# Kernel tuning notes

Hardware: AMD Instinct MI355X
Metric: run time of the kernel (lower is better)

Reference implementation:

```python
import jax, jax.numpy as jnp
import numpy as np

SOM_H, SOM_W = 16, 16
K = SOM_H * SOM_W          # num_embeddings = 256
EMB_D = 32                 # embedding_dim
ALPHA, BETA = 6.0, 1.0


def _build_tables():
    """Static SOM grid neighbor tables (rectangular geometry).
    ind[k] is a 0/1 row over the K codebook entries marking k and its
    up/down/left/right grid neighbors; counts[k] = number of neighbors incl self.
    Replaces the original per-voxel Python loop with a constant lookup table.
    """
    ind = np.zeros((K, K), np.float32)
    for idx in range(K):
        h, w = divmod(idx, SOM_W)
        neigh = [idx]
        if h - 1 >= 0:
            neigh.append((h - 1) * SOM_W + w)
        if h + 1 < SOM_H:
            neigh.append((h + 1) * SOM_W + w)
        if w - 1 >= 0:
            neigh.append(h * SOM_W + (w - 1))
        if w + 1 < SOM_W:
            neigh.append(h * SOM_W + (w + 1))
        ind[idx, neigh] = 1.0
    counts = ind.sum(axis=1)
    return jnp.asarray(ind), jnp.asarray(counts)

_IND_TABLE, _COUNTS = _build_tables()


def setup_inputs() -> dict:
    key = jax.random.key(0)
    k1, k2 = jax.random.split(key)
    x = jax.random.normal(k1, (8, EMB_D, 32, 32, 32), dtype=jnp.float32)  # [B,C,D,H,W]
    W = jax.random.normal(k2, (K, EMB_D), dtype=jnp.float32)              # codebook
    return {"x": x, "W": W}


def reference(x, W):
    # channels-last: [B, D, H, Wd, C]
    inputs = jnp.transpose(x, (0, 2, 3, 4, 1))
    in_shape = inputs.shape
    flat = inputs.reshape(-1, EMB_D)                    # [N, d]
    flat_sg = jax.lax.stop_gradient(flat)               # matches flat_inputs.detach()

    # squared Euclidean distances to all codebook entries: [N, K]
    dist = (jnp.sum(flat_sg ** 2, axis=1, keepdims=True)
            + jnp.sum(W ** 2, axis=1)
            - 2.0 * flat_sg @ W.T)

    enc_idx = jnp.argmin(dist, axis=1)                  # [N]
    encodings = jax.nn.one_hot(enc_idx, K, dtype=inputs.dtype)  # [N, K]

    quantized = (encodings @ W).reshape(in_shape)
    commitment_loss = jnp.mean((quantized - inputs) ** 2)

    # vectorized neighbor indicator + counts via static table gather
    indicator = _IND_TABLE[enc_idx]                     # [N, K], constant wrt floats
    total_neighbors = jnp.sum(_COUNTS[enc_idx])
    somloss = jnp.sum(dist * indicator) / total_neighbors

    loss = ALPHA * commitment_loss + BETA * somloss

    # straight-through estimator
    quantized_st = inputs + jax.lax.stop_gradient(quantized - inputs)
    out = jnp.transpose(quantized_st, (0, 4, 1, 2, 3))  # back to [B,C,D,H,W]
    return loss, out, encodings
```

## Files before the change

### kernel.cpp

```cpp
#include <hip/hip_runtime.h>


#define SOM_K      256
#define EMB_D      32
#define WPAD       36
#define N_VOX      262144
#define SPATIAL    32768
#define OUT_ELEMS  8388608
#define COMMIT_DEN 8388608.0f
#define NSLOT      256

#define CONST_AS __attribute__((address_space(4)))

__global__ __launch_bounds__(256) void som_prep_kernel(float* __restrict__ ws) {
  float4* p = (float4*)ws;
  int t = threadIdx.x;
#pragma unroll
  for (int i = 0; i < 4; ++i) p[i * 256 + t] = make_float4(0.f, 0.f, 0.f, 0.f);
}

__global__ __launch_bounds__(256, 4) void som_main_kernel(
    const float* __restrict__ x,
    const float* __restrict__ w,
    float* __restrict__ slots,
    float* __restrict__ out,
    float* __restrict__ enc) {
  __shared__ __align__(16) float wl[SOM_K * WPAD];
  __shared__ __align__(16) float wsql[SOM_K];

  const int t = threadIdx.x;
  const CONST_AS float* wcp = (const CONST_AS float*)(unsigned long long)w;

  const int n    = blockIdx.x * 256 + t;
  const int base = (n >> 15) * (EMB_D * SPATIAL) + (n & (SPATIAL - 1));
  float xv[EMB_D];
#pragma unroll
  for (int c = 0; c < EMB_D; ++c) xv[c] = x[base + c * SPATIAL];

#pragma unroll
  for (int i = 0; i < 32; ++i) {
    int e = i * 256 + t;
    int r = e >> 5, c = e & 31;
    wl[r * WPAD + c] = w[e];
  }
  __syncthreads();

  {
    const float4* row = (const float4*)(wl + t * WPAD);
    float s = 0.0f;
#pragma unroll
    for (int j = 0; j < 8; ++j) {
      float4 q = row[j];
      s = fmaf(q.x, q.x, s);
      s = fmaf(q.y, q.y, s);
      s = fmaf(q.z, q.z, s);
      s = fmaf(q.w, q.w, s);
    }
    wsql[t] = s;
  }

  float xsq = 0.0f;
#pragma unroll
  for (int c = 0; c < EMB_D; ++c) xsq = fmaf(xv[c], xv[c], xsq);
  __syncthreads();

  {
    const int lane = t & 63, wave = t >> 6;
    float* rb = enc + (size_t)(blockIdx.x * 256 + wave * 64) * SOM_K;
    float4* rb4 = (float4*)(rb + 3);
    const float4 z4 = make_float4(0.f, 0.f, 0.f, 0.f);
    for (int r = 0; r < 63; ++r) rb4[r * 64 + lane] = z4;
    if (lane < 63) rb4[4032 + lane] = z4;
    if (lane == 0)       { rb[0] = 0.f; rb[1] = 0.f; rb[2] = 0.f; }
    else if (lane == 63) { rb[16383] = 0.f; }
  }

  float best = 3.402823466e38f;
  int   bidx = 0;
  const float4* wsq4 = (const float4*)wsql;
#pragma unroll 1
  for (int k = 0; k < SOM_K; k += 4) {
    const CONST_AS float* r0 = wcp + (k << 5);
    const CONST_AS float* r1 = r0 + 32;
    const CONST_AS float* r2 = r0 + 64;
    const CONST_AS float* r3 = r0 + 96;
    float d0 = 0.0f, d1 = 0.0f, d2 = 0.0f, d3 = 0.0f;
#pragma unroll
    for (int j = 0; j < EMB_D; ++j) {
      const float xj = xv[j];
      d0 = fmaf(r0[j], xj, d0);
      d1 = fmaf(r1[j], xj, d1);
      d2 = fmaf(r2[j], xj, d2);
      d3 = fmaf(r3[j], xj, d3);
    }
    const float4 ws4 = wsq4[k >> 2];
    const float e0 = (xsq + ws4.x) - 2.0f * d0;
    const float e1 = (xsq + ws4.y) - 2.0f * d1;
    const float e2 = (xsq + ws4.z) - 2.0f * d2;
    const float e3 = (xsq + ws4.w) - 2.0f * d3;
    if (e0 < best) { best = e0; bidx = k;     }
    if (e1 < best) { best = e1; bidx = k + 1; }
    if (e2 < best) { best = e2; bidx = k + 2; }
    if (e3 < best) { best = e3; bidx = k + 3; }
  }

  asm volatile("s_waitcnt vmcnt(0)" ::: "memory");
  enc[(size_t)n * SOM_K + bidx] = 1.0f;

  float commit = 0.0f;
  {
    const float4* qrow = (const float4*)(wl + bidx * WPAD);
#pragma unroll
    for (int j = 0; j < 8; ++j) {
      float4 q = qrow[j];
      float qq[4] = { q.x, q.y, q.z, q.w };
#pragma unroll
      for (int u = 0; u < 4; ++u) {
        int c = 4 * j + u;
        out[base + c * SPATIAL] = qq[u];
        float df = qq[u] - xv[c];
        commit = fmaf(df, df, commit);
      }
    }
  }

  float som = best;
  float cnt = 1.0f;
  {
    const int h   = bidx >> 4;
    const int wc2 = bidx & 15;
    const int   cand[4]  = { bidx - 16, bidx + 16, bidx - 1, bidx + 1 };
    const float valid[4] = { h > 0 ? 1.f : 0.f,  h < 15 ? 1.f : 0.f,
                             wc2 > 0 ? 1.f : 0.f, wc2 < 15 ? 1.f : 0.f };
#pragma unroll
    for (int j = 0; j < 4; ++j) {
      int nk = valid[j] != 0.0f ? cand[j] : bidx;
      const float4* nrow = (const float4*)(wl + nk * WPAD);
      float dot = 0.0f;
#pragma unroll
      for (int jj = 0; jj < 8; ++jj) {
        float4 q = nrow[jj];
        dot = fmaf(q.x, xv[4 * jj + 0], dot);
        dot = fmaf(q.y, xv[4 * jj + 1], dot);
        dot = fmaf(q.z, xv[4 * jj + 2], dot);
        dot = fmaf(q.w, xv[4 * jj + 3], dot);
      }
      float d = (xsq + wsql[nk]) - 2.0f * dot;
      som = fmaf(valid[j], d, som);
      cnt += valid[j];
    }
  }

  for (int off = 32; off > 0; off >>= 1) {
    commit += __shfl_down(commit, off, 64);
    som    += __shfl_down(som,    off, 64);
    cnt    += __shfl_down(cnt,    off, 64);
  }
  if ((t & 63) == 0) {
    float* sp = slots + (size_t)(blockIdx.x & (NSLOT - 1)) * 16;
    atomicAdd(sp + 0, commit);
    atomicAdd(sp + 1, som);
    atomicAdd(sp + 2, cnt);
  }
}

__global__ __launch_bounds__(64) void som_final_kernel(
    const float* __restrict__ slots, float* __restrict__ loss) {
  const int t = threadIdx.x;
  float commit = 0.f, som = 0.f, cnt = 0.f;
#pragma unroll
  for (int i = 0; i < 4; ++i) {
    const float* sp = slots + (size_t)(i * 64 + t) * 16;
    commit += sp[0]; som += sp[1]; cnt += sp[2];
  }
  for (int off = 32; off > 0; off >>= 1) {
    commit += __shfl_down(commit, off, 64);
    som    += __shfl_down(som,    off, 64);
    cnt    += __shfl_down(cnt,    off, 64);
  }
  if (t == 0) loss[0] = 6.0f * (commit / COMMIT_DEN) + som / cnt;
}

extern "C" void kernel_launch(void* const* d_in, const int* in_sizes, int n_in,
                              void* d_out, int out_size, void* d_ws, size_t ws_size,
                              hipStream_t stream) {
  const float* x = (const float*)d_in[0];
  const float* w = (const float*)d_in[1];
  float* ws  = (float*)d_ws;
  float* o   = (float*)d_out;

  som_prep_kernel<<<1, 256, 0, stream>>>(ws);
  som_main_kernel<<<N_VOX / 256, 256, 0, stream>>>(
      x, w, ws, o + 1, o + 1 + OUT_ELEMS);
  som_final_kernel<<<1, 64, 0, stream>>>(ws, o);
}
```

Measured before the change: 402.7 us.

## Split each voxel's codebook search across two threads and drop the LDS codebook copy

Each block now runs 512 threads, and each voxel is handled by a thread pair. Each thread of the pair scans half of the 256 codebook entries, and the two results are merged with a lane shuffle that breaks ties toward the lower index. The shared-memory copy of the codebook is removed; the quantized row and the SOM neighbor distances are read directly from global memory, with the neighbor work and output channels split between the two threads. The aim is more parallelism and shorter per-thread argmin loops. The cost is that codebook reads no longer use the constant/scalar address space and become per-lane vector memory loads, and both threads of a pair load the full input vector.

```diff
diff --git a/kernel.cpp b/kernel.cpp
--- a/kernel.cpp
+++ b/kernel.cpp
@@ -3,15 +3,12 @@
 
 #define SOM_K      256
 #define EMB_D      32
-#define WPAD       36
 #define N_VOX      262144
 #define SPATIAL    32768
 #define OUT_ELEMS  8388608
 #define COMMIT_DEN 8388608.0f
 #define NSLOT      256
 
-#define CONST_AS __attribute__((address_space(4)))
-
 __global__ __launch_bounds__(256) void som_prep_kernel(float* __restrict__ ws) {
   float4* p = (float4*)ws;
   int t = threadIdx.x;
@@ -19,42 +16,30 @@
   for (int i = 0; i < 4; ++i) p[i * 256 + t] = make_float4(0.f, 0.f, 0.f, 0.f);
 }
 
-__global__ __launch_bounds__(256, 4) void som_main_kernel(
+__global__ __launch_bounds__(512, 8) void som_main_kernel(
     const float* __restrict__ x,
     const float* __restrict__ w,
     float* __restrict__ slots,
     float* __restrict__ out,
     float* __restrict__ enc) {
-  __shared__ __align__(16) float wl[SOM_K * WPAD];
   __shared__ __align__(16) float wsql[SOM_K];
 
-  const int t = threadIdx.x;
-  const CONST_AS float* wcp = (const CONST_AS float*)(unsigned long long)w;
-
-  const int n    = blockIdx.x * 256 + t;
+  const int t    = threadIdx.x;
+  const int half = t & 1;
+  const int vloc = t >> 1;
+  const int n    = blockIdx.x * 256 + vloc;
   const int base = (n >> 15) * (EMB_D * SPATIAL) + (n & (SPATIAL - 1));
+
   float xv[EMB_D];
 #pragma unroll
   for (int c = 0; c < EMB_D; ++c) xv[c] = x[base + c * SPATIAL];
 
-#pragma unroll
-  for (int i = 0; i < 32; ++i) {
-    int e = i * 256 + t;
-    int r = e >> 5, c = e & 31;
-    wl[r * WPAD + c] = w[e];
-  }
-  __syncthreads();
-
-  {
-    const float4* row = (const float4*)(wl + t * WPAD);
+  if (t < SOM_K) {
     float s = 0.0f;
 #pragma unroll
-    for (int j = 0; j < 8; ++j) {
-      float4 q = row[j];
-      s = fmaf(q.x, q.x, s);
-      s = fmaf(q.y, q.y, s);
-      s = fmaf(q.z, q.z, s);
-      s = fmaf(q.w, q.w, s);
+    for (int c = 0; c < EMB_D; ++c) {
+      float v = w[t * EMB_D + c];
+      s = fmaf(v, v, s);
     }
     wsql[t] = s;
   }
@@ -66,24 +51,28 @@
 
   {
     const int lane = t & 63, wave = t >> 6;
-    float* rb = enc + (size_t)(blockIdx.x * 256 + wave * 64) * SOM_K;
+    float* rb = enc + (size_t)(blockIdx.x * 256 + wave * 32) * SOM_K;
     float4* rb4 = (float4*)(rb + 3);
     const float4 z4 = make_float4(0.f, 0.f, 0.f, 0.f);
-    for (int r = 0; r < 63; ++r) rb4[r * 64 + lane] = z4;
-    if (lane < 63) rb4[4032 + lane] = z4;
+    for (int r = 0; r < 32; ++r) {
+      int idx = r * 64 + lane;
+      if (idx < 2047) rb4[idx] = z4;
+    }
     if (lane == 0)       { rb[0] = 0.f; rb[1] = 0.f; rb[2] = 0.f; }
-    else if (lane == 63) { rb[16383] = 0.f; }
-  }
-
+    else if (lane == 63) { rb[8191] = 0.f; }
+  }
+
+  const int klo = half << 7;
+  const float* __restrict__ wrb = w + (klo << 5);
+  const float4* wsq4 = (const float4*)wsql;
   float best = 3.402823466e38f;
-  int   bidx = 0;
-  const float4* wsq4 = (const float4*)wsql;
+  int   bidx = klo;
 #pragma unroll 1
-  for (int k = 0; k < SOM_K; k += 4) {
-    const CONST_AS float* r0 = wcp + (k << 5);
-    const CONST_AS float* r1 = r0 + 32;
-    const CONST_AS float* r2 = r0 + 64;
-    const CONST_AS float* r3 = r0 + 96;
+  for (int k = 0; k < 128; k += 4) {
+    const float* r0 = wrb + (k << 5);
+    const float* r1 = r0 + 32;
+    const float* r2 = r0 + 64;
+    const float* r3 = r0 + 96;
     float d0 = 0.0f, d1 = 0.0f, d2 = 0.0f, d3 = 0.0f;
 #pragma unroll
     for (int j = 0; j < EMB_D; ++j) {
@@ -93,25 +82,35 @@
       d2 = fmaf(r2[j], xj, d2);
       d3 = fmaf(r3[j], xj, d3);
     }
-    const float4 ws4 = wsq4[k >> 2];
+    const float4 ws4 = wsq4[(klo + k) >> 2];
     const float e0 = (xsq + ws4.x) - 2.0f * d0;
     const float e1 = (xsq + ws4.y) - 2.0f * d1;
     const float e2 = (xsq + ws4.z) - 2.0f * d2;
     const float e3 = (xsq + ws4.w) - 2.0f * d3;
-    if (e0 < best) { best = e0; bidx = k;     }
-    if (e1 < best) { best = e1; bidx = k + 1; }
-    if (e2 < best) { best = e2; bidx = k + 2; }
-    if (e3 < best) { best = e3; bidx = k + 3; }
+    if (e0 < best) { best = e0; bidx = klo + k;     }
+    if (e1 < best) { best = e1; bidx = klo + k + 1; }
+    if (e2 < best) { best = e2; bidx = klo + k + 2; }
+    if (e3 < best) { best = e3; bidx = klo + k + 3; }
+  }
+
+  {
+    const float eo = __shfl_xor(best, 1, 64);
+    const int   ko = __shfl_xor(bidx, 1, 64);
+    if (half == 0) { if (eo < best)    { best = eo; bidx = ko; } }
+    else           { if (!(best < eo)) { best = eo; bidx = ko; } }
   }
 
   asm volatile("s_waitcnt vmcnt(0)" ::: "memory");
-  enc[(size_t)n * SOM_K + bidx] = 1.0f;
+  if (half == 0) enc[(size_t)n * SOM_K + bidx] = 1.0f;
 
   float commit = 0.0f;
   {
-    const float4* qrow = (const float4*)(wl + bidx * WPAD);
-#pragma unroll
-    for (int j = 0; j < 8; ++j) {
+    const float4* wv4  = (const float4*)w;
+    const float4* qrow = wv4 + (bidx << 3);
+    const int j0 = half * 4;
+#pragma unroll
+    for (int jj = 0; jj < 4; ++jj) {
+      const int j = j0 + jj;
       float4 q = qrow[j];
       float qq[4] = { q.x, q.y, q.z, q.w };
 #pragma unroll
@@ -124,18 +123,25 @@
     }
   }
 
-  float som = best;
-  float cnt = 1.0f;
+  float som = (half == 0) ? best : 0.0f;
+  float cnt = (half == 0) ? 1.0f : 0.0f;
   {
     const int h   = bidx >> 4;
     const int wc2 = bidx & 15;
-    const int   cand[4]  = { bidx - 16, bidx + 16, bidx - 1, bidx + 1 };
-    const float valid[4] = { h > 0 ? 1.f : 0.f,  h < 15 ? 1.f : 0.f,
-                             wc2 > 0 ? 1.f : 0.f, wc2 < 15 ? 1.f : 0.f };
-#pragma unroll
-    for (int j = 0; j < 4; ++j) {
+    int   cand[2];
+    float valid[2];
+    if (half == 0) {
+      cand[0] = bidx - 16; valid[0] = h > 0  ? 1.f : 0.f;
+      cand[1] = bidx + 16; valid[1] = h < 15 ? 1.f : 0.f;
+    } else {
+      cand[0] = bidx - 1;  valid[0] = wc2 > 0  ? 1.f : 0.f;
+      cand[1] = bidx + 1;  valid[1] = wc2 < 15 ? 1.f : 0.f;
+    }
+    const float4* wv4 = (const float4*)w;
+#pragma unroll
+    for (int j = 0; j < 2; ++j) {
       int nk = valid[j] != 0.0f ? cand[j] : bidx;
-      const float4* nrow = (const float4*)(wl + nk * WPAD);
+      const float4* nrow = wv4 + (nk << 3);
       float dot = 0.0f;
 #pragma unroll
       for (int jj = 0; jj < 8; ++jj) {
@@ -190,7 +196,7 @@
   float* o   = (float*)d_out;
 
   som_prep_kernel<<<1, 256, 0, stream>>>(ws);
-  som_main_kernel<<<N_VOX / 256, 256, 0, stream>>>(
+  som_main_kernel<<<N_VOX / 256, 512, 0, stream>>>(
       x, w, ws, o + 1, o + 1 + OUT_ELEMS);
   som_final_kernel<<<1, 64, 0, stream>>>(ws, o);
 }
```

Result: slower. 842.4 us (+109.2%).
